# Optimization experiments

Measured on AMD Instinct MI355X. Metric: run time of the kernel, lower is better.

## Reference

```python
import jax, jax.numpy as jnp
from jax import lax
import numpy as np

B, T, I, H, O = 128, 256, 256, 1024, 128


def _rnn_layer(x, W_ih, W_hh, b_ih, b_hh):
    # x: [B, T, D_in] -> hidden states [B, T, H]
    # precompute input projection for all timesteps (batched GEMM)
    xW = jnp.einsum('btd,hd->bth', x, W_ih) + b_ih + b_hh  # [B, T, H]

    def step(h, xw_t):
        h = jnp.tanh(xw_t + h @ W_hh.T)  # [B, H]
        return h, h

    h0 = jnp.zeros((x.shape[0], W_hh.shape[0]), x.dtype)
    _, hs = lax.scan(step, h0, jnp.swapaxes(xW, 0, 1))  # hs: [T, B, H]
    return jnp.swapaxes(hs, 0, 1)  # [B, T, H]


def setup_inputs() -> dict:
    key = jax.random.key(0)
    ks = jax.random.split(key, 11)
    s_ih0 = 1.0 / np.sqrt(H)
    inp = {
        'X': jax.random.normal(ks[0], (B, T, I), jnp.float32),
        'W_ih0': jax.random.uniform(ks[1], (H, I), jnp.float32, -s_ih0, s_ih0),
        'W_hh0': jax.random.uniform(ks[2], (H, H), jnp.float32, -s_ih0, s_ih0),
        'b_ih0': jax.random.uniform(ks[3], (H,), jnp.float32, -s_ih0, s_ih0),
        'b_hh0': jax.random.uniform(ks[4], (H,), jnp.float32, -s_ih0, s_ih0),
        'W_ih1': jax.random.uniform(ks[5], (H, H), jnp.float32, -s_ih0, s_ih0),
        'W_hh1': jax.random.uniform(ks[6], (H, H), jnp.float32, -s_ih0, s_ih0),
        'b_ih1': jax.random.uniform(ks[7], (H,), jnp.float32, -s_ih0, s_ih0),
        'b_hh1': jax.random.uniform(ks[8], (H,), jnp.float32, -s_ih0, s_ih0),
        'W_fc': jax.random.uniform(ks[9], (O, H), jnp.float32, -s_ih0, s_ih0),
        'b_fc': jax.random.uniform(ks[10], (O,), jnp.float32, -s_ih0, s_ih0),
    }
    return inp


def reference(X, W_ih0, W_hh0, b_ih0, b_hh0, W_ih1, W_hh1, b_ih1, b_hh1, W_fc, b_fc):
    h1 = _rnn_layer(X, W_ih0, W_hh0, b_ih0, b_hh0)   # layer 0: [B, T, H]
    h2 = _rnn_layer(h1, W_ih1, W_hh1, b_ih1, b_hh1)  # layer 1: [B, T, H]
    last = h2[:, -1, :]                               # [B, H]
    return last @ W_fc.T + b_fc                       # [B, O]
```

## Files before the change

### kernel.cpp

```cpp
#include <hip/hip_runtime.h>
#include <stdint.h>
#include <stddef.h>

#define B_ 128
#define T_ 256
#define I_ 256
#define H_ 1024
#define O_ 128

typedef __attribute__((ext_vector_type(8))) __bf16 bf16x8;
typedef __attribute__((ext_vector_type(4))) float f32x4;
typedef unsigned long long u64;



__global__ void split_kernel(const float* __restrict__ src, __bf16* __restrict__ hi,
                             __bf16* __restrict__ lo, int n) {
    int i = blockIdx.x * blockDim.x + threadIdx.x;
    int stride = gridDim.x * blockDim.x;
    for (; i < n; i += stride) {
        float v = src[i];
        __bf16 h = (__bf16)v;
        hi[i] = h;
        lo[i] = (__bf16)(v - (float)h);
    }
}

__global__ void pack_x(const float* __restrict__ X, u64* __restrict__ xp) {
    int i = blockIdx.x * 256 + threadIdx.x;
    int ln = i & 15;
    int k2 = (i >> 4) & 127;
    int bt16 = (i >> 11) & 7;
    int t = i >> 14;
    int b = bt16 * 16 + ln;
    long xo = (long)b * T_ * I_ + (long)t * I_ + k2 * 2;
    float v0 = X[xo], v1 = X[xo + 1];
    union { __bf16 b; unsigned short u; } h0, l0, h1, l1;
    h0.b = (__bf16)v0; l0.b = (__bf16)(v0 - (float)h0.b);
    h1.b = (__bf16)v1; l1.b = (__bf16)(v1 - (float)h1.b);
    u64 pk = (u64)((unsigned)h0.u | ((unsigned)l0.u << 16))
           | ((u64)((unsigned)h1.u | ((unsigned)l1.u << 16)) << 32);
    xp[(long)t * 16384 + bt16 * 2048 + k2 * 16 + ln] = pk;
}

__global__ void bias_sum_kernel(const float* __restrict__ a, const float* __restrict__ b,
                                float* __restrict__ o, int n) {
    int i = blockIdx.x * blockDim.x + threadIdx.x;
    if (i < n) o[i] = a[i] + b[i];
}

__global__ void transpose_fc(const float* __restrict__ w, float* __restrict__ wt) {
    int i = blockIdx.x * blockDim.x + threadIdx.x;
    if (i < O_ * H_) {
        int o = i / H_, k = i - o * H_;
        wt[k * O_ + o] = w[i];
    }
}


__device__ __forceinline__ void unpack4(const u64* d, bf16x8* hi, bf16x8* lo) {
    union { unsigned u[4]; bf16x8 v; } Hh, Ll;
    #pragma unroll
    for (int i = 0; i < 4; ++i) {
        unsigned lo32 = (unsigned)d[i], hi32 = (unsigned)(d[i] >> 32);
        Hh.u[i] = (lo32 & 0xFFFFu) | (hi32 << 16);
        Ll.u[i] = (lo32 >> 16) | (hi32 & 0xFFFF0000u);
    }
    *hi = Hh.v; *lo = Ll.v;
}

template <int CPW, int SEG0CH, bool CACHED0>
__device__ __forceinline__ void step_full(
    const u64* __restrict__ A0,
    const u64* __restrict__ Sp,
    const bf16x8 (&wh)[CPW][2], const bf16x8 (&wl)[CPW][2],
    const float* __restrict__ bs,
    u64* __restrict__ So,
    int bt, int jt, int w, float* red)
{
    const int lane = threadIdx.x & 63;
    const int ln = lane & 15;
    const int q  = lane >> 4;

    f32x4 acc[2][2][3];
    #pragma unroll
    for (int s = 0; s < 2; ++s)
        #pragma unroll
        for (int n = 0; n < 2; ++n)
            #pragma unroll
            for (int r = 0; r < 3; ++r)
                acc[s][n][r] = (f32x4){0.f, 0.f, 0.f, 0.f};

    constexpr int PF = 2;
    u64 d[PF][2][4];

    auto issue = [&](int c, u64 (&dst)[2][4]) {
        const int gC = w * CPW + c;
        if (gC < SEG0CH) {
            const u64* base = A0 + (long)(gC * 16 + q * 4) * 16 + ln;
            #pragma unroll
            for (int s = 0; s < 2; ++s) {
                const u64* p = base + (long)(bt * 2 + s) * (SEG0CH * 256);
                #pragma unroll
                for (int i = 0; i < 4; ++i) {
                    if (CACHED0) dst[s][i] = p[i * 16];
                    else dst[s][i] = __hip_atomic_load((u64*)p + i * 16,
                                         __ATOMIC_RELAXED, __HIP_MEMORY_SCOPE_AGENT);
                }
            }
        } else {
            const u64* base = Sp + (long)((gC - SEG0CH) * 16 + q * 4) * 16 + ln;
            #pragma unroll
            for (int s = 0; s < 2; ++s) {
                const u64* p = base + (long)(bt * 2 + s) * 8192;
                #pragma unroll
                for (int i = 0; i < 4; ++i)
                    dst[s][i] = __hip_atomic_load((u64*)p + i * 16,
                                    __ATOMIC_RELAXED, __HIP_MEMORY_SCOPE_AGENT);
            }
        }
    };

    issue(0, d[0]);
    issue(1, d[1]);

    #pragma unroll
    for (int c = 0; c < CPW; ++c) {
        bf16x8 ah[2], al[2];
        #pragma unroll
        for (int s = 0; s < 2; ++s)
            unpack4(d[c & 1][s], &ah[s], &al[s]);
        if (c + PF < CPW) issue(c + PF, d[c & 1]);
        #pragma unroll
        for (int s = 0; s < 2; ++s)
            #pragma unroll
            for (int n = 0; n < 2; ++n) {
                acc[s][n][0] = __builtin_amdgcn_mfma_f32_16x16x32_bf16(ah[s], wh[c][n], acc[s][n][0], 0, 0, 0);
                acc[s][n][1] = __builtin_amdgcn_mfma_f32_16x16x32_bf16(al[s], wh[c][n], acc[s][n][1], 0, 0, 0);
                acc[s][n][2] = __builtin_amdgcn_mfma_f32_16x16x32_bf16(ah[s], wl[c][n], acc[s][n][2], 0, 0, 0);
            }
    }

    {
        float* my = red + w * 1056;
        #pragma unroll
        for (int s = 0; s < 2; ++s)
            #pragma unroll
            for (int n = 0; n < 2; ++n) {
                f32x4 sum = acc[s][n][0] + acc[s][n][1] + acc[s][n][2];
                #pragma unroll
                for (int r = 0; r < 4; ++r)
                    my[(s * 16 + q * 4 + r) * 33 + n * 16 + ln] = sum[r];
            }
    }
    __syncthreads();

    {
        int tid = threadIdx.x;
        int row = tid & 31;
        int jp  = tid >> 5;
        int c0 = jp * 2;
        float v0 = 0.f, v1 = 0.f;
        #pragma unroll
        for (int w8 = 0; w8 < 8; ++w8) {
            v0 += red[w8 * 1056 + row * 33 + c0];
            v1 += red[w8 * 1056 + row * 33 + c0 + 1];
        }
        int j0 = jt * 32 + c0;
        float h0 = tanhf(v0 + bs[j0]);
        float h1v = tanhf(v1 + bs[j0 + 1]);
        union { __bf16 b; unsigned short u; } x0h, x0l, x1h, x1l;
        x0h.b = (__bf16)h0;  x0l.b = (__bf16)(h0 - (float)x0h.b);
        x1h.b = (__bf16)h1v; x1l.b = (__bf16)(h1v - (float)x1h.b);
        u64 pk = (u64)((unsigned)x0h.u | ((unsigned)x0l.u << 16))
               | ((u64)((unsigned)x1h.u | ((unsigned)x1l.u << 16)) << 32);
        long idx = (long)(bt * 2 + (row >> 4)) * 8192 + (long)(jt * 16 + jp) * 16 + (row & 15);
        __hip_atomic_store(&So[idx], pk, __ATOMIC_RELAXED, __HIP_MEMORY_SCOPE_AGENT);
    }
}

__device__ __forceinline__ void domain_barrier(unsigned* bar, int dom, unsigned step) {
    asm volatile("s_waitcnt vmcnt(0)" ::: "memory");
    __syncthreads();
    if (threadIdx.x == 0) {
        unsigned* cnt = &bar[dom * 64];
        unsigned* rel = &bar[dom * 64 + 32];
        unsigned old = __hip_atomic_fetch_add(cnt, 1u, __ATOMIC_RELAXED,
                                              __HIP_MEMORY_SCOPE_AGENT);
        if (old == step * 64u + 63u)
            __hip_atomic_store(rel, step + 1u, __ATOMIC_RELAXED,
                               __HIP_MEMORY_SCOPE_AGENT);
        while (__hip_atomic_load(rel, __ATOMIC_RELAXED,
                                 __HIP_MEMORY_SCOPE_AGENT) <= step)
            __builtin_amdgcn_s_sleep(2);
    }
    __syncthreads();
    asm volatile("" ::: "memory");
}

struct PArgs {
    const u64* xp;
    const __bf16 *Wi0h, *Wi0l, *Wr0h, *Wr0l;
    const __bf16 *Wi1h, *Wi1l, *Wr1h, *Wr1l;
    const float *bs0, *bs1;
    u64 *s0a, *s0b, *s1a, *s1b;
    unsigned* bar;
};

__global__ __launch_bounds__(512, 2) void persistent_rnn(PArgs a) {
    __shared__ float red[8 * 1056];
    const int w = threadIdx.x >> 6;
    const int lane = threadIdx.x & 63;
    const int ln = lane & 15;
    const int q  = lane >> 4;
    const int layer = blockIdx.x >> 7;
    const int r7 = blockIdx.x & 127;
    const int jt = r7 & 31;
    const int bt = r7 >> 5;

    if (layer == 0) {
        bf16x8 wh[5][2], wl[5][2];
        #pragma unroll
        for (int c = 0; c < 5; ++c) {
            int gC = w * 5 + c;
            #pragma unroll
            for (int n = 0; n < 2; ++n) {
                int jr = jt * 32 + n * 16 + ln;
                if (gC < 8) {
                    wh[c][n] = *(const bf16x8*)(a.Wi0h + (long)jr * 256 + gC * 32 + q * 8);
                    wl[c][n] = *(const bf16x8*)(a.Wi0l + (long)jr * 256 + gC * 32 + q * 8);
                } else {
                    wh[c][n] = *(const bf16x8*)(a.Wr0h + (long)jr * 1024 + (gC - 8) * 32 + q * 8);
                    wl[c][n] = *(const bf16x8*)(a.Wr0l + (long)jr * 1024 + (gC - 8) * 32 + q * 8);
                }
            }
        }
        for (int t = 0; t <= T_; ++t) {
            if (t < T_) {
                const u64* sin = (t & 1) ? a.s0b : a.s0a;
                u64* sout      = (t & 1) ? a.s0a : a.s0b;
                step_full<5, 8, true>(a.xp + (long)t * 16384, sin, wh, wl, a.bs0,
                                      sout, bt, jt, w, red);
            }
            domain_barrier(a.bar, bt, (unsigned)t);
        }
    } else {
        bf16x8 wh[8][2], wl[8][2];
        #pragma unroll
        for (int c = 0; c < 8; ++c) {
            int gC = w * 8 + c;
            #pragma unroll
            for (int n = 0; n < 2; ++n) {
                int jr = jt * 32 + n * 16 + ln;
                if (gC < 32) {
                    wh[c][n] = *(const bf16x8*)(a.Wi1h + (long)jr * 1024 + gC * 32 + q * 8);
                    wl[c][n] = *(const bf16x8*)(a.Wi1l + (long)jr * 1024 + gC * 32 + q * 8);
                } else {
                    wh[c][n] = *(const bf16x8*)(a.Wr1h + (long)jr * 1024 + (gC - 32) * 32 + q * 8);
                    wl[c][n] = *(const bf16x8*)(a.Wr1l + (long)jr * 1024 + (gC - 32) * 32 + q * 8);
                }
            }
        }
        for (int t = 0; t <= T_; ++t) {
            if (t >= 1) {
                int t1 = t - 1;
                const u64* h1in = (t1 & 1) ? a.s0a : a.s0b;
                const u64* sin  = (t1 & 1) ? a.s1b : a.s1a;
                u64* sout       = (t1 & 1) ? a.s1a : a.s1b;
                step_full<8, 32, false>(h1in, sin, wh, wl, a.bs1,
                                        sout, bt, jt, w, red);
            }
            domain_barrier(a.bar, bt, (unsigned)t);
        }
    }
}

__global__ __launch_bounds__(128) void fc_kernel(const u64* __restrict__ sp,
                                                 const float* __restrict__ wt,
                                                 const float* __restrict__ bfc,
                                                 float* __restrict__ out) {
    int b = blockIdx.x;
    int o = threadIdx.x;
    int bt = b >> 4, r = b & 15;
    float acc = 0.f;
    #pragma unroll 4
    for (int k2 = 0; k2 < H_ / 2; ++k2) {
        u64 pk = __hip_atomic_load((u64*)sp + (long)bt * 8192 + (long)k2 * 16 + r,
                                   __ATOMIC_RELAXED, __HIP_MEMORY_SCOPE_AGENT);
        union { unsigned short u; __bf16 bf; } hh, hl;
        unsigned lo32 = (unsigned)pk, hi32 = (unsigned)(pk >> 32);
        hh.u = (unsigned short)(lo32 & 0xFFFF); hl.u = (unsigned short)(lo32 >> 16);
        float x0 = (float)hh.bf + (float)hl.bf;
        hh.u = (unsigned short)(hi32 & 0xFFFF); hl.u = (unsigned short)(hi32 >> 16);
        float x1 = (float)hh.bf + (float)hl.bf;
        acc += x0 * wt[(2 * k2) * O_ + o] + x1 * wt[(2 * k2 + 1) * O_ + o];
    }
    out[b * O_ + o] = acc + bfc[o];
}


extern "C" void kernel_launch(void* const* d_in, const int* in_sizes, int n_in,
                              void* d_out, int out_size, void* d_ws, size_t ws_size,
                              hipStream_t stream) {
    const float* X     = (const float*)d_in[0];
    const float* Wih0  = (const float*)d_in[1];
    const float* Whh0  = (const float*)d_in[2];
    const float* bih0  = (const float*)d_in[3];
    const float* bhh0  = (const float*)d_in[4];
    const float* Wih1  = (const float*)d_in[5];
    const float* Whh1  = (const float*)d_in[6];
    const float* bih1  = (const float*)d_in[7];
    const float* bhh1  = (const float*)d_in[8];
    const float* Wfc   = (const float*)d_in[9];
    const float* bfc   = (const float*)d_in[10];
    float* out = (float*)d_out;

    char* p = (char*)d_ws;
    auto alloc = [&](size_t bytes) -> void* {
        void* r = (void*)p;
        p += (bytes + 255) & ~(size_t)255;
        return r;
    };
    const size_t nW0 = (size_t)H_ * I_;
    const size_t nW  = (size_t)H_ * H_;
    u64* xp      = (u64*)alloc((size_t)T_ * 16384 * 8);
    __bf16* W0h  = (__bf16*)alloc(nW0 * 2);
    __bf16* W0l  = (__bf16*)alloc(nW0 * 2);
    __bf16* Wh0h = (__bf16*)alloc(nW * 2);
    __bf16* Wh0l = (__bf16*)alloc(nW * 2);
    __bf16* Wi1h = (__bf16*)alloc(nW * 2);
    __bf16* Wi1l = (__bf16*)alloc(nW * 2);
    __bf16* Wh1h = (__bf16*)alloc(nW * 2);
    __bf16* Wh1l = (__bf16*)alloc(nW * 2);
    u64* s0a  = (u64*)alloc(65536 * 8);
    u64* s0b  = (u64*)alloc(65536 * 8);
    u64* s1a  = (u64*)alloc(65536 * 8);
    u64* s1b  = (u64*)alloc(65536 * 8);
    float* wfct = (float*)alloc((size_t)H_ * O_ * 4);
    float* bs0  = (float*)alloc((size_t)H_ * 4);
    float* bs1  = (float*)alloc((size_t)H_ * 4);
    unsigned* bar = (unsigned*)alloc(4096);
    (void)ws_size; (void)n_in; (void)in_sizes; (void)out_size;

    pack_x<<<16384, 256, 0, stream>>>(X, xp);
    split_kernel<<<512, 256, 0, stream>>>(Wih0, W0h, W0l, (int)nW0);
    split_kernel<<<1024, 256, 0, stream>>>(Whh0, Wh0h, Wh0l, (int)nW);
    split_kernel<<<1024, 256, 0, stream>>>(Wih1, Wi1h, Wi1l, (int)nW);
    split_kernel<<<1024, 256, 0, stream>>>(Whh1, Wh1h, Wh1l, (int)nW);
    bias_sum_kernel<<<4, 256, 0, stream>>>(bih0, bhh0, bs0, H_);
    bias_sum_kernel<<<4, 256, 0, stream>>>(bih1, bhh1, bs1, H_);
    transpose_fc<<<(O_ * H_ + 255) / 256, 256, 0, stream>>>(Wfc, wfct);

    hipMemsetAsync(s0a, 0, 65536 * 8, stream);
    hipMemsetAsync(s1a, 0, 65536 * 8, stream);
    hipMemsetAsync(bar, 0, 4096, stream);

    PArgs args;
    args.xp = xp;
    args.Wi0h = W0h; args.Wi0l = W0l; args.Wr0h = Wh0h; args.Wr0l = Wh0l;
    args.Wi1h = Wi1h; args.Wi1l = Wi1l; args.Wr1h = Wh1h; args.Wr1l = Wh1l;
    args.bs0 = bs0; args.bs1 = bs1;
    args.s0a = s0a; args.s0b = s0b; args.s1a = s1a; args.s1b = s1b;
    args.bar = bar;
    void* kp[] = { &args };
    hipLaunchCooperativeKernel((void*)persistent_rnn, dim3(256), dim3(512), kp, 0, stream);

    fc_kernel<<<B_, O_, 0, stream>>>(s1a, wfct, bfc, out);
}
```

Baseline: 1.971 ms.

## Halve persistent grid; each block handles two batch tiles with split barriers

The persistent RNN kernel now launches 128 blocks instead of 256, and each block processes two batch tiles (btA, btB) per timestep using the same register-resident weights. The barrier is split into arrive and wait phases, so one domain's barrier latency can overlap with computing the other domain. This aims to halve weight register loads per batch and hide the barrier spin time. The cost is half the parallelism: each block does twice the serial work per step, so per-step latency may grow.

```diff
diff --git a/kernel.cpp b/kernel.cpp
--- a/kernel.cpp
+++ b/kernel.cpp
@@ -179,19 +179,22 @@
     }
 }
 
-__device__ __forceinline__ void domain_barrier(unsigned* bar, int dom, unsigned step) {
+__device__ __forceinline__ void bar_arrive(unsigned* bar, int dom, unsigned round) {
     asm volatile("s_waitcnt vmcnt(0)" ::: "memory");
     __syncthreads();
     if (threadIdx.x == 0) {
-        unsigned* cnt = &bar[dom * 64];
-        unsigned* rel = &bar[dom * 64 + 32];
-        unsigned old = __hip_atomic_fetch_add(cnt, 1u, __ATOMIC_RELAXED,
+        unsigned old = __hip_atomic_fetch_add(&bar[dom * 64], 1u, __ATOMIC_RELAXED,
                                               __HIP_MEMORY_SCOPE_AGENT);
-        if (old == step * 64u + 63u)
-            __hip_atomic_store(rel, step + 1u, __ATOMIC_RELAXED,
+        if (old == round * 64u + 63u)
+            __hip_atomic_store(&bar[dom * 64 + 32], round + 1u, __ATOMIC_RELAXED,
                                __HIP_MEMORY_SCOPE_AGENT);
-        while (__hip_atomic_load(rel, __ATOMIC_RELAXED,
-                                 __HIP_MEMORY_SCOPE_AGENT) <= step)
+    }
+}
+
+__device__ __forceinline__ void bar_wait(unsigned* bar, int dom, unsigned round) {
+    if (threadIdx.x == 0) {
+        while (__hip_atomic_load(&bar[dom * 64 + 32], __ATOMIC_RELAXED,
+                                 __HIP_MEMORY_SCOPE_AGENT) < round)
             __builtin_amdgcn_s_sleep(2);
     }
     __syncthreads();
@@ -213,10 +216,11 @@
     const int lane = threadIdx.x & 63;
     const int ln = lane & 15;
     const int q  = lane >> 4;
-    const int layer = blockIdx.x >> 7;
-    const int r7 = blockIdx.x & 127;
-    const int jt = r7 & 31;
-    const int bt = r7 >> 5;
+    const int layer = blockIdx.x >> 6;
+    const int r6 = blockIdx.x & 63;
+    const int jt = r6 & 31;
+    const int pr = r6 >> 5;
+    const int btA = pr * 2, btB = pr * 2 + 1;
 
     if (layer == 0) {
         bf16x8 wh[5][2], wl[5][2];
@@ -235,14 +239,16 @@
                 }
             }
         }
-        for (int t = 0; t <= T_; ++t) {
-            if (t < T_) {
-                const u64* sin = (t & 1) ? a.s0b : a.s0a;
-                u64* sout      = (t & 1) ? a.s0a : a.s0b;
-                step_full<5, 8, true>(a.xp + (long)t * 16384, sin, wh, wl, a.bs0,
-                                      sout, bt, jt, w, red);
-            }
-            domain_barrier(a.bar, bt, (unsigned)t);
+        for (int t = 0; t < T_; ++t) {
+            const u64* sin = (t & 1) ? a.s0b : a.s0a;
+            u64* sout      = (t & 1) ? a.s0a : a.s0b;
+            const u64* xt  = a.xp + (long)t * 16384;
+            if (t) bar_wait(a.bar, btA, (unsigned)t);
+            step_full<5, 8, true>(xt, sin, wh, wl, a.bs0, sout, btA, jt, w, red);
+            bar_arrive(a.bar, btA, (unsigned)t);
+            if (t) bar_wait(a.bar, btB, (unsigned)t);
+            step_full<5, 8, true>(xt, sin, wh, wl, a.bs0, sout, btB, jt, w, red);
+            bar_arrive(a.bar, btB, (unsigned)t);
         }
     } else {
         bf16x8 wh[8][2], wl[8][2];
@@ -261,16 +267,19 @@
                 }
             }
         }
-        for (int t = 0; t <= T_; ++t) {
-            if (t >= 1) {
-                int t1 = t - 1;
-                const u64* h1in = (t1 & 1) ? a.s0a : a.s0b;
-                const u64* sin  = (t1 & 1) ? a.s1b : a.s1a;
-                u64* sout       = (t1 & 1) ? a.s1a : a.s1b;
-                step_full<8, 32, false>(h1in, sin, wh, wl, a.bs1,
-                                        sout, bt, jt, w, red);
-            }
-            domain_barrier(a.bar, bt, (unsigned)t);
+        bar_arrive(a.bar, btA, 0u);
+        bar_arrive(a.bar, btB, 0u);
+        for (int t = 1; t <= T_; ++t) {
+            int t1 = t - 1;
+            const u64* h1in = (t1 & 1) ? a.s0a : a.s0b;
+            const u64* sin  = (t1 & 1) ? a.s1b : a.s1a;
+            u64* sout       = (t1 & 1) ? a.s1a : a.s1b;
+            bar_wait(a.bar, btA, (unsigned)t);
+            step_full<8, 32, false>(h1in, sin, wh, wl, a.bs1, sout, btA, jt, w, red);
+            bar_arrive(a.bar, btA, (unsigned)t);
+            bar_wait(a.bar, btB, (unsigned)t);
+            step_full<8, 32, false>(h1in, sin, wh, wl, a.bs1, sout, btB, jt, w, red);
+            bar_arrive(a.bar, btB, (unsigned)t);
         }
     }
 }
@@ -363,7 +372,7 @@
     args.s0a = s0a; args.s0b = s0b; args.s1a = s1a; args.s1b = s1b;
     args.bar = bar;
     void* kp[] = { &args };
-    hipLaunchCooperativeKernel((void*)persistent_rnn, dim3(256), dim3(512), kp, 0, stream);
+    hipLaunchCooperativeKernel((void*)persistent_rnn, dim3(128), dim3(512), kp, 0, stream);
 
     fc_kernel<<<B_, O_, 0, stream>>>(s1a, wfct, bfc, out);
 }
```

After: 3.476 ms. 76.4% more time.

## Split hi/lo planes, decouple layer barriers, merge low-order MFMA accumulators

Applied to the files above, without the earlier changes.

Stores activations and inputs as separate hi and lo bf16 planes laid out as MFMA fragments. This removes the per-step unpacking shuffle and allows vector 16-byte loads. Replaces the shared per-domain barrier with separate arrive/wait counters per layer, so layer 0 and layer 1 blocks synchronise only on their true dependencies and can run with looser coupling. The two low-order MFMA products now share one accumulator, which saves registers and the final add. The changed synchronisation protocol adds risk of ordering or race bugs.

```diff
diff --git a/kernel.cpp b/kernel.cpp
--- a/kernel.cpp
+++ b/kernel.cpp
@@ -26,21 +26,28 @@
     }
 }
 
-__global__ void pack_x(const float* __restrict__ X, u64* __restrict__ xp) {
+__global__ void pack_x(const float* __restrict__ X, __bf16* __restrict__ xh,
+                       __bf16* __restrict__ xl) {
     int i = blockIdx.x * 256 + threadIdx.x;
-    int ln = i & 15;
-    int k2 = (i >> 4) & 127;
-    int bt16 = (i >> 11) & 7;
-    int t = i >> 14;
-    int b = bt16 * 16 + ln;
-    long xo = (long)b * T_ * I_ + (long)t * I_ + k2 * 2;
-    float v0 = X[xo], v1 = X[xo + 1];
-    union { __bf16 b; unsigned short u; } h0, l0, h1, l1;
-    h0.b = (__bf16)v0; l0.b = (__bf16)(v0 - (float)h0.b);
-    h1.b = (__bf16)v1; l1.b = (__bf16)(v1 - (float)h1.b);
-    u64 pk = (u64)((unsigned)h0.u | ((unsigned)l0.u << 16))
-           | ((u64)((unsigned)h1.u | ((unsigned)l1.u << 16)) << 32);
-    xp[(long)t * 16384 + bt16 * 2048 + k2 * 16 + ln] = pk;
+    int lnidx = i & 15;
+    int kg   = (i >> 4) & 31;
+    int bgrp = (i >> 9) & 7;
+    int t    = i >> 12;
+    int b = bgrp * 16 + lnidx;
+    const float* xs = X + (long)b * T_ * I_ + (long)t * I_ + kg * 8;
+    float4 f0 = *(const float4*)xs;
+    float4 f1 = *(const float4*)(xs + 4);
+    float f[8] = {f0.x, f0.y, f0.z, f0.w, f1.x, f1.y, f1.z, f1.w};
+    bf16x8 hv, lv;
+    #pragma unroll
+    for (int j = 0; j < 8; ++j) {
+        __bf16 h = (__bf16)f[j];
+        hv[j] = h;
+        lv[j] = (__bf16)(f[j] - (float)h);
+    }
+    long o = (long)t * 32768 + (long)(bgrp * 32 + kg) * 128 + lnidx * 8;
+    *(bf16x8*)(xh + o) = hv;
+    *(bf16x8*)(xl + o) = lv;
 }
 
 __global__ void bias_sum_kernel(const float* __restrict__ a, const float* __restrict__ b,
@@ -57,87 +64,80 @@
     }
 }
 
-
-__device__ __forceinline__ void unpack4(const u64* d, bf16x8* hi, bf16x8* lo) {
-    union { unsigned u[4]; bf16x8 v; } Hh, Ll;
-    #pragma unroll
-    for (int i = 0; i < 4; ++i) {
-        unsigned lo32 = (unsigned)d[i], hi32 = (unsigned)(d[i] >> 32);
-        Hh.u[i] = (lo32 & 0xFFFFu) | (hi32 << 16);
-        Ll.u[i] = (lo32 >> 16) | (hi32 & 0xFFFF0000u);
-    }
-    *hi = Hh.v; *lo = Ll.v;
-}
+union Frag { u64 d[2]; bf16x8 v; };
 
 template <int CPW, int SEG0CH, bool CACHED0>
 __device__ __forceinline__ void step_full(
-    const u64* __restrict__ A0,
-    const u64* __restrict__ Sp,
+    const __bf16* __restrict__ A0h, const __bf16* __restrict__ A0l,
+    const __bf16* __restrict__ Sh,  const __bf16* __restrict__ Sl,
     const bf16x8 (&wh)[CPW][2], const bf16x8 (&wl)[CPW][2],
     const float* __restrict__ bs,
-    u64* __restrict__ So,
+    __bf16* __restrict__ Soh, __bf16* __restrict__ Sol,
     int bt, int jt, int w, float* red)
 {
     const int lane = threadIdx.x & 63;
     const int ln = lane & 15;
     const int q  = lane >> 4;
 
-    f32x4 acc[2][2][3];
+    f32x4 acc[2][2][2];
     #pragma unroll
     for (int s = 0; s < 2; ++s)
         #pragma unroll
         for (int n = 0; n < 2; ++n)
             #pragma unroll
-            for (int r = 0; r < 3; ++r)
+            for (int r = 0; r < 2; ++r)
                 acc[s][n][r] = (f32x4){0.f, 0.f, 0.f, 0.f};
 
-    constexpr int PF = 2;
-    u64 d[PF][2][4];
-
-    auto issue = [&](int c, u64 (&dst)[2][4]) {
+    Frag SH[2][2], SL[2][2];
+
+    auto issue = [&](int c, Frag (&FH)[2], Frag (&FL)[2]) {
         const int gC = w * CPW + c;
         if (gC < SEG0CH) {
-            const u64* base = A0 + (long)(gC * 16 + q * 4) * 16 + ln;
             #pragma unroll
             for (int s = 0; s < 2; ++s) {
-                const u64* p = base + (long)(bt * 2 + s) * (SEG0CH * 256);
-                #pragma unroll
-                for (int i = 0; i < 4; ++i) {
-                    if (CACHED0) dst[s][i] = p[i * 16];
-                    else dst[s][i] = __hip_atomic_load((u64*)p + i * 16,
-                                         __ATOMIC_RELAXED, __HIP_MEMORY_SCOPE_AGENT);
+                long off = ((long)(bt * 2 + s) * (SEG0CH * 4) + gC * 4 + q) * 128 + ln * 8;
+                if constexpr (CACHED0) {
+                    FH[s].v = *(const bf16x8*)(A0h + off);
+                    FL[s].v = *(const bf16x8*)(A0l + off);
+                } else {
+                    const u64* ph = (const u64*)(A0h + off);
+                    const u64* pl = (const u64*)(A0l + off);
+                    FH[s].d[0] = __hip_atomic_load(ph,     __ATOMIC_RELAXED, __HIP_MEMORY_SCOPE_AGENT);
+                    FH[s].d[1] = __hip_atomic_load(ph + 1, __ATOMIC_RELAXED, __HIP_MEMORY_SCOPE_AGENT);
+                    FL[s].d[0] = __hip_atomic_load(pl,     __ATOMIC_RELAXED, __HIP_MEMORY_SCOPE_AGENT);
+                    FL[s].d[1] = __hip_atomic_load(pl + 1, __ATOMIC_RELAXED, __HIP_MEMORY_SCOPE_AGENT);
                 }
             }
         } else {
-            const u64* base = Sp + (long)((gC - SEG0CH) * 16 + q * 4) * 16 + ln;
             #pragma unroll
             for (int s = 0; s < 2; ++s) {
-                const u64* p = base + (long)(bt * 2 + s) * 8192;
-                #pragma unroll
-                for (int i = 0; i < 4; ++i)
-                    dst[s][i] = __hip_atomic_load((u64*)p + i * 16,
-                                    __ATOMIC_RELAXED, __HIP_MEMORY_SCOPE_AGENT);
+                long off = ((long)(bt * 2 + s) * 128 + (gC - SEG0CH) * 4 + q) * 128 + ln * 8;
+                const u64* ph = (const u64*)(Sh + off);
+                const u64* pl = (const u64*)(Sl + off);
+                FH[s].d[0] = __hip_atomic_load(ph,     __ATOMIC_RELAXED, __HIP_MEMORY_SCOPE_AGENT);
+                FH[s].d[1] = __hip_atomic_load(ph + 1, __ATOMIC_RELAXED, __HIP_MEMORY_SCOPE_AGENT);
+                FL[s].d[0] = __hip_atomic_load(pl,     __ATOMIC_RELAXED, __HIP_MEMORY_SCOPE_AGENT);
+                FL[s].d[1] = __hip_atomic_load(pl + 1, __ATOMIC_RELAXED, __HIP_MEMORY_SCOPE_AGENT);
             }
         }
     };
 
-    issue(0, d[0]);
-    issue(1, d[1]);
+    issue(0, SH[0], SL[0]);
+    issue(1, SH[1], SL[1]);
 
     #pragma unroll
     for (int c = 0; c < CPW; ++c) {
         bf16x8 ah[2], al[2];
         #pragma unroll
-        for (int s = 0; s < 2; ++s)
-            unpack4(d[c & 1][s], &ah[s], &al[s]);
-        if (c + PF < CPW) issue(c + PF, d[c & 1]);
+        for (int s = 0; s < 2; ++s) { ah[s] = SH[c & 1][s].v; al[s] = SL[c & 1][s].v; }
+        if (c + 2 < CPW) issue(c + 2, SH[c & 1], SL[c & 1]);
         #pragma unroll
         for (int s = 0; s < 2; ++s)
             #pragma unroll
             for (int n = 0; n < 2; ++n) {
                 acc[s][n][0] = __builtin_amdgcn_mfma_f32_16x16x32_bf16(ah[s], wh[c][n], acc[s][n][0], 0, 0, 0);
                 acc[s][n][1] = __builtin_amdgcn_mfma_f32_16x16x32_bf16(al[s], wh[c][n], acc[s][n][1], 0, 0, 0);
-                acc[s][n][2] = __builtin_amdgcn_mfma_f32_16x16x32_bf16(ah[s], wl[c][n], acc[s][n][2], 0, 0, 0);
+                acc[s][n][1] = __builtin_amdgcn_mfma_f32_16x16x32_bf16(ah[s], wl[c][n], acc[s][n][1], 0, 0, 0);
             }
     }
 
@@ -147,7 +147,7 @@
         for (int s = 0; s < 2; ++s)
             #pragma unroll
             for (int n = 0; n < 2; ++n) {
-                f32x4 sum = acc[s][n][0] + acc[s][n][1] + acc[s][n][2];
+                f32x4 sum = acc[s][n][0] + acc[s][n][1];
                 #pragma unroll
                 for (int r = 0; r < 4; ++r)
                     my[(s * 16 + q * 4 + r) * 33 + n * 16 + ln] = sum[r];
@@ -172,26 +172,31 @@
         union { __bf16 b; unsigned short u; } x0h, x0l, x1h, x1l;
         x0h.b = (__bf16)h0;  x0l.b = (__bf16)(h0 - (float)x0h.b);
         x1h.b = (__bf16)h1v; x1l.b = (__bf16)(h1v - (float)x1h.b);
-        u64 pk = (u64)((unsigned)x0h.u | ((unsigned)x0l.u << 16))
-               | ((u64)((unsigned)x1h.u | ((unsigned)x1l.u << 16)) << 32);
-        long idx = (long)(bt * 2 + (row >> 4)) * 8192 + (long)(jt * 16 + jp) * 16 + (row & 15);
-        __hip_atomic_store(&So[idx], pk, __ATOMIC_RELAXED, __HIP_MEMORY_SCOPE_AGENT);
-    }
-}
-
-__device__ __forceinline__ void domain_barrier(unsigned* bar, int dom, unsigned step) {
+        unsigned uh = (unsigned)x0h.u | ((unsigned)x1h.u << 16);
+        unsigned ul = (unsigned)x0l.u | ((unsigned)x1l.u << 16);
+        long idx = ((long)(bt * 2 + (row >> 4)) * 128 + jt * 4 + (c0 >> 3)) * 128
+                 + (row & 15) * 8 + (c0 & 7);
+        __hip_atomic_store((unsigned*)(Soh + idx), uh, __ATOMIC_RELAXED, __HIP_MEMORY_SCOPE_AGENT);
+        __hip_atomic_store((unsigned*)(Sol + idx), ul, __ATOMIC_RELAXED, __HIP_MEMORY_SCOPE_AGENT);
+    }
+}
+
+__device__ __forceinline__ void bar_arrive(unsigned* bar, int slot, unsigned k) {
     asm volatile("s_waitcnt vmcnt(0)" ::: "memory");
     __syncthreads();
     if (threadIdx.x == 0) {
-        unsigned* cnt = &bar[dom * 64];
-        unsigned* rel = &bar[dom * 64 + 32];
-        unsigned old = __hip_atomic_fetch_add(cnt, 1u, __ATOMIC_RELAXED,
+        unsigned old = __hip_atomic_fetch_add(&bar[slot * 64], 1u, __ATOMIC_RELAXED,
                                               __HIP_MEMORY_SCOPE_AGENT);
-        if (old == step * 64u + 63u)
-            __hip_atomic_store(rel, step + 1u, __ATOMIC_RELAXED,
+        if (old == k * 32u + 31u)
+            __hip_atomic_store(&bar[slot * 64 + 32], k + 1u, __ATOMIC_RELAXED,
                                __HIP_MEMORY_SCOPE_AGENT);
-        while (__hip_atomic_load(rel, __ATOMIC_RELAXED,
-                                 __HIP_MEMORY_SCOPE_AGENT) <= step)
+    }
+}
+
+__device__ __forceinline__ void bar_wait(unsigned* bar, int slot, unsigned v) {
+    if (threadIdx.x == 0) {
+        while (__hip_atomic_load(&bar[slot * 64 + 32], __ATOMIC_RELAXED,
+                                 __HIP_MEMORY_SCOPE_AGENT) < v)
             __builtin_amdgcn_s_sleep(2);
     }
     __syncthreads();
@@ -199,11 +204,12 @@
 }
 
 struct PArgs {
-    const u64* xp;
+    const __bf16 *xh, *xl;
     const __bf16 *Wi0h, *Wi0l, *Wr0h, *Wr0l;
     const __bf16 *Wi1h, *Wi1l, *Wr1h, *Wr1l;
     const float *bs0, *bs1;
-    u64 *s0a, *s0b, *s1a, *s1b;
+    __bf16 *s0ah, *s0al, *s0bh, *s0bl;
+    __bf16 *s1ah, *s1al, *s1bh, *s1bl;
     unsigned* bar;
 };
 
@@ -217,6 +223,8 @@
     const int r7 = blockIdx.x & 127;
     const int jt = r7 & 31;
     const int bt = r7 >> 5;
+    const int slotL0 = 0 * 4 + bt;
+    const int slotL1 = 1 * 4 + bt;
 
     if (layer == 0) {
         bf16x8 wh[5][2], wl[5][2];
@@ -235,14 +243,17 @@
                 }
             }
         }
-        for (int t = 0; t <= T_; ++t) {
-            if (t < T_) {
-                const u64* sin = (t & 1) ? a.s0b : a.s0a;
-                u64* sout      = (t & 1) ? a.s0a : a.s0b;
-                step_full<5, 8, true>(a.xp + (long)t * 16384, sin, wh, wl, a.bs0,
-                                      sout, bt, jt, w, red);
-            }
-            domain_barrier(a.bar, bt, (unsigned)t);
+        for (int t = 0; t < T_; ++t) {
+            const __bf16* sinh_ = (t & 1) ? a.s0bh : a.s0ah;
+            const __bf16* sinl_ = (t & 1) ? a.s0bl : a.s0al;
+            __bf16* south      = (t & 1) ? a.s0ah : a.s0bh;
+            __bf16* soutl      = (t & 1) ? a.s0al : a.s0bl;
+            if (t >= 1) bar_wait(a.bar, slotL0, (unsigned)t);
+            if (t >= 2) bar_wait(a.bar, slotL1, (unsigned)(t - 1));
+            step_full<5, 8, true>(a.xh + (long)t * 32768, a.xl + (long)t * 32768,
+                                  sinh_, sinl_, wh, wl, a.bs0,
+                                  south, soutl, bt, jt, w, red);
+            bar_arrive(a.bar, slotL0, (unsigned)t);
         }
     } else {
         bf16x8 wh[8][2], wl[8][2];
@@ -261,39 +272,41 @@
                 }
             }
         }
-        for (int t = 0; t <= T_; ++t) {
-            if (t >= 1) {
-                int t1 = t - 1;
-                const u64* h1in = (t1 & 1) ? a.s0a : a.s0b;
-                const u64* sin  = (t1 & 1) ? a.s1b : a.s1a;
-                u64* sout       = (t1 & 1) ? a.s1a : a.s1b;
-                step_full<8, 32, false>(h1in, sin, wh, wl, a.bs1,
-                                        sout, bt, jt, w, red);
-            }
-            domain_barrier(a.bar, bt, (unsigned)t);
-        }
-    }
-}
-
-__global__ __launch_bounds__(128) void fc_kernel(const u64* __restrict__ sp,
+        for (int r = 1; r <= T_; ++r) {
+            int t1 = r - 1;
+            const __bf16* h1h = (t1 & 1) ? a.s0ah : a.s0bh;
+            const __bf16* h1l = (t1 & 1) ? a.s0al : a.s0bl;
+            const __bf16* sinh_ = (t1 & 1) ? a.s1bh : a.s1ah;
+            const __bf16* sinl_ = (t1 & 1) ? a.s1bl : a.s1al;
+            __bf16* south       = (t1 & 1) ? a.s1ah : a.s1bh;
+            __bf16* soutl       = (t1 & 1) ? a.s1al : a.s1bl;
+            bar_wait(a.bar, slotL0, (unsigned)r);
+            if (r >= 2) bar_wait(a.bar, slotL1, (unsigned)(r - 1));
+            step_full<8, 32, false>(h1h, h1l, sinh_, sinl_, wh, wl, a.bs1,
+                                    south, soutl, bt, jt, w, red);
+            bar_arrive(a.bar, slotL1, (unsigned)(r - 1));
+        }
+    }
+}
+
+__global__ __launch_bounds__(128) void fc_kernel(const __bf16* __restrict__ sph,
+                                                 const __bf16* __restrict__ spl,
                                                  const float* __restrict__ wt,
                                                  const float* __restrict__ bfc,
                                                  float* __restrict__ out) {
     int b = blockIdx.x;
     int o = threadIdx.x;
-    int bt = b >> 4, r = b & 15;
     float acc = 0.f;
-    #pragma unroll 4
-    for (int k2 = 0; k2 < H_ / 2; ++k2) {
-        u64 pk = __hip_atomic_load((u64*)sp + (long)bt * 8192 + (long)k2 * 16 + r,
-                                   __ATOMIC_RELAXED, __HIP_MEMORY_SCOPE_AGENT);
-        union { unsigned short u; __bf16 bf; } hh, hl;
-        unsigned lo32 = (unsigned)pk, hi32 = (unsigned)(pk >> 32);
-        hh.u = (unsigned short)(lo32 & 0xFFFF); hl.u = (unsigned short)(lo32 >> 16);
-        float x0 = (float)hh.bf + (float)hl.bf;
-        hh.u = (unsigned short)(hi32 & 0xFFFF); hl.u = (unsigned short)(hi32 >> 16);
-        float x1 = (float)hh.bf + (float)hl.bf;
-        acc += x0 * wt[(2 * k2) * O_ + o] + x1 * wt[(2 * k2 + 1) * O_ + o];
+    #pragma unroll 2
+    for (int kg = 0; kg < 128; ++kg) {
+        long off = ((long)(b >> 4) * 128 + kg) * 128 + (b & 15) * 8;
+        bf16x8 hv = *(const bf16x8*)(sph + off);
+        bf16x8 lv = *(const bf16x8*)(spl + off);
+        #pragma unroll
+        for (int j = 0; j < 8; ++j) {
+            float x = (float)hv[j] + (float)lv[j];
+            acc += x * wt[(kg * 8 + j) * O_ + o];
+        }
     }
     out[b * O_ + o] = acc + bfc[o];
 }
@@ -323,7 +336,9 @@
     };
     const size_t nW0 = (size_t)H_ * I_;
     const size_t nW  = (size_t)H_ * H_;
-    u64* xp      = (u64*)alloc((size_t)T_ * 16384 * 8);
+    const size_t planeSt = (size_t)131072;
+    __bf16* xh   = (__bf16*)alloc((size_t)T_ * 32768 * 2);
+    __bf16* xl   = (__bf16*)alloc((size_t)T_ * 32768 * 2);
     __bf16* W0h  = (__bf16*)alloc(nW0 * 2);
     __bf16* W0l  = (__bf16*)alloc(nW0 * 2);
     __bf16* Wh0h = (__bf16*)alloc(nW * 2);
@@ -332,17 +347,21 @@
     __bf16* Wi1l = (__bf16*)alloc(nW * 2);
     __bf16* Wh1h = (__bf16*)alloc(nW * 2);
     __bf16* Wh1l = (__bf16*)alloc(nW * 2);
-    u64* s0a  = (u64*)alloc(65536 * 8);
-    u64* s0b  = (u64*)alloc(65536 * 8);
-    u64* s1a  = (u64*)alloc(65536 * 8);
-    u64* s1b  = (u64*)alloc(65536 * 8);
+    __bf16* s0ah = (__bf16*)alloc(planeSt * 2);
+    __bf16* s0al = (__bf16*)alloc(planeSt * 2);
+    __bf16* s0bh = (__bf16*)alloc(planeSt * 2);
+    __bf16* s0bl = (__bf16*)alloc(planeSt * 2);
+    __bf16* s1ah = (__bf16*)alloc(planeSt * 2);
+    __bf16* s1al = (__bf16*)alloc(planeSt * 2);
+    __bf16* s1bh = (__bf16*)alloc(planeSt * 2);
+    __bf16* s1bl = (__bf16*)alloc(planeSt * 2);
     float* wfct = (float*)alloc((size_t)H_ * O_ * 4);
     float* bs0  = (float*)alloc((size_t)H_ * 4);
     float* bs1  = (float*)alloc((size_t)H_ * 4);
     unsigned* bar = (unsigned*)alloc(4096);
     (void)ws_size; (void)n_in; (void)in_sizes; (void)out_size;
 
-    pack_x<<<16384, 256, 0, stream>>>(X, xp);
+    pack_x<<<4096, 256, 0, stream>>>(X, xh, xl);
     split_kernel<<<512, 256, 0, stream>>>(Wih0, W0h, W0l, (int)nW0);
     split_kernel<<<1024, 256, 0, stream>>>(Whh0, Wh0h, Wh0l, (int)nW);
     split_kernel<<<1024, 256, 0, stream>>>(Wih1, Wi1h, Wi1l, (int)nW);
@@ -351,19 +370,22 @@
     bias_sum_kernel<<<4, 256, 0, stream>>>(bih1, bhh1, bs1, H_);
     transpose_fc<<<(O_ * H_ + 255) / 256, 256, 0, stream>>>(Wfc, wfct);
 
-    hipMemsetAsync(s0a, 0, 65536 * 8, stream);
-    hipMemsetAsync(s1a, 0, 65536 * 8, stream);
+    hipMemsetAsync(s0ah, 0, planeSt * 2, stream);
+    hipMemsetAsync(s0al, 0, planeSt * 2, stream);
+    hipMemsetAsync(s1ah, 0, planeSt * 2, stream);
+    hipMemsetAsync(s1al, 0, planeSt * 2, stream);
     hipMemsetAsync(bar, 0, 4096, stream);
 
     PArgs args;
-    args.xp = xp;
+    args.xh = xh; args.xl = xl;
     args.Wi0h = W0h; args.Wi0l = W0l; args.Wr0h = Wh0h; args.Wr0l = Wh0l;
     args.Wi1h = Wi1h; args.Wi1l = Wi1l; args.Wr1h = Wh1h; args.Wr1l = Wh1l;
     args.bs0 = bs0; args.bs1 = bs1;
-    args.s0a = s0a; args.s0b = s0b; args.s1a = s1a; args.s1b = s1b;
+    args.s0ah = s0ah; args.s0al = s0al; args.s0bh = s0bh; args.s0bl = s0bl;
+    args.s1ah = s1ah; args.s1al = s1al; args.s1bh = s1bh; args.s1bl = s1bl;
     args.bar = bar;
     void* kp[] = { &args };
     hipLaunchCooperativeKernel((void*)persistent_rnn, dim3(256), dim3(512), kp, 0, stream);
 
-    fc_kernel<<<B_, O_, 0, stream>>>(s1a, wfct, bfc, out);
-}
+    fc_kernel<<<B_, O_, 0, stream>>>(s1ah, s1al, wfct, bfc, out);
+}
```

Result: slower. 2.265 ms (+14.9%).
